# Optimization experiments

Hardware: AMD Instinct MI355X
Metric: run time of the kernel (lower is better)

Reference implementation:

```python
import jax, jax.numpy as jnp
import numpy as np

N_NODES = 500_000
N_EDGES = 16_000_000
C_IN = 1
C_OUT = 4


def gcn_conv(x, edge_index, W, b):
    """PyG GCNConv: add self-loops, symmetric normalization, linear + scatter-add.
    x: [N, Cin], edge_index: [2, E] (src, dst), W: [Cin, Cout], b: [Cout].
    """
    n = x.shape[0]
    loops = jnp.arange(n, dtype=edge_index.dtype)
    src = jnp.concatenate([edge_index[0], loops])  # [E+N]
    dst = jnp.concatenate([edge_index[1], loops])  # [E+N]
    h = x @ W  # [N, Cout]
    # degree at target nodes (with self-loops)
    deg = jax.ops.segment_sum(jnp.ones_like(dst, dtype=h.dtype), dst, num_segments=n)
    dinv = jnp.where(deg > 0, jax.lax.rsqrt(deg), 0.0)  # deg^{-1/2}
    norm = dinv[src] * dinv[dst]  # [E+N]
    msgs = norm[:, None] * h[src]  # [E+N, Cout] gathered + scaled messages
    out = jax.ops.segment_sum(msgs, dst, num_segments=n)  # scatter-add at targets
    return out + b


def setup_inputs() -> dict:
    key = jax.random.key(0)
    k0, k1, k2, k3 = jax.random.split(key, 4)
    x = jax.random.normal(k0, (N_NODES, C_IN), dtype=jnp.float32)
    edge_index = jax.random.randint(k1, (2, N_EDGES), 0, N_NODES, dtype=jnp.int64)
    W1 = jax.random.normal(k2, (C_IN, C_OUT), dtype=jnp.float32) / np.sqrt(C_IN)
    b1 = jnp.zeros((C_OUT,), dtype=jnp.float32)
    W2 = jax.random.normal(k3, (C_OUT, C_OUT), dtype=jnp.float32) / np.sqrt(C_OUT)
    b2 = jnp.zeros((C_OUT,), dtype=jnp.float32)
    return {"x": x, "edge_index": edge_index, "W1": W1, "b1": b1, "W2": W2, "b2": b2}


def reference(x, edge_index, W1, b1, W2, b2):
    h = jax.nn.relu(gcn_conv(x, edge_index, W1, b1))
    return gcn_conv(h, edge_index, W2, b2)
```

## Files before the change

kernel.cpp:

```cpp
#include <hip/hip_runtime.h>


#define B1_BLOCKS 512
#define B1_THREADS 1024
#define TILE1 16384
#define B2_THREADS 1024
#define TILE2 16384
#define MAXNB1 256
#define SORT_STAGE 12032
#define FB_BLOCKS 512
#define FB_THREADS 1024
#define FB_PAD 8
#define MAXNBF 2048

__global__ __launch_bounds__(B1_THREADS) void k_bin1(
    const int* __restrict__ src, const int* __restrict__ dst, int E,
    int chunk, int nb1, int C1, int* __restrict__ gcur1,
    int* __restrict__ pay1) {
  __shared__ int out[TILE1];
  __shared__ int hist[MAXNB1], toff[MAXNB1], wcur[MAXNB1], gb[MAXNB1];
  __shared__ int sbuf[2][MAXNB1];
  const int tid = threadIdx.x;
  const long long e0 = (long long)blockIdx.x * chunk;
  long long reml = (long long)E - e0;
  const int lim = reml < 0 ? 0 : (reml < chunk ? (int)reml : chunk);
  const int* dch = dst + e0;
  const int* sch = src + e0;

  for (int tb = 0; tb < lim; tb += TILE1) {
    const int tcnt = min(TILE1, lim - tb);
    const int nv = tcnt >> 2;
    for (int j = tid; j < MAXNB1; j += B1_THREADS) hist[j] = 0;
    __syncthreads();

    const int* dt = dch + tb;
    for (int k = tid; k < nv; k += B1_THREADS) {
      int4 d = reinterpret_cast<const int4*>(dt)[k];
      atomicAdd(&hist[d.x >> 11], 1);
      atomicAdd(&hist[d.y >> 11], 1);
      atomicAdd(&hist[d.z >> 11], 1);
      atomicAdd(&hist[d.w >> 11], 1);
    }
    for (int k = (nv << 2) + tid; k < tcnt; k += B1_THREADS)
      atomicAdd(&hist[dt[k] >> 11], 1);
    __syncthreads();

    if (tid < MAXNB1) sbuf[0][tid] = hist[tid];
    __syncthreads();
    int pi = 0;
    for (int dd = 1; dd < MAXNB1; dd <<= 1) {
      if (tid < MAXNB1) {
        int v = sbuf[pi][tid];
        if (tid >= dd) v += sbuf[pi][tid - dd];
        sbuf[pi ^ 1][tid] = v;
      }
      pi ^= 1;
      __syncthreads();
    }
    if (tid < MAXNB1) {
      int c = hist[tid];
      int exc = sbuf[pi][tid] - c;
      toff[tid] = exc;
      wcur[tid] = exc;
      gb[tid] = c ? atomicAdd(&gcur1[tid], c) : 0;
    }
    __syncthreads();

    const int* st = sch + tb;
    for (int k = tid; k < nv; k += B1_THREADS) {
      int4 d = reinterpret_cast<const int4*>(dt)[k];
      int4 s = reinterpret_cast<const int4*>(st)[k];
      int r0 = atomicAdd(&wcur[d.x >> 11], 1);
      int r1 = atomicAdd(&wcur[d.y >> 11], 1);
      int r2 = atomicAdd(&wcur[d.z >> 11], 1);
      int r3 = atomicAdd(&wcur[d.w >> 11], 1);
      out[r0] = (s.x << 11) | (d.x & 2047);
      out[r1] = (s.y << 11) | (d.y & 2047);
      out[r2] = (s.z << 11) | (d.z & 2047);
      out[r3] = (s.w << 11) | (d.w & 2047);
    }
    for (int k = (nv << 2) + tid; k < tcnt; k += B1_THREADS) {
      int d = dt[k], s = st[k];
      int r = atomicAdd(&wcur[d >> 11], 1);
      out[r] = (s << 11) | (d & 2047);
    }
    __syncthreads();

    const int wv = tid >> 6, lane = tid & 63;
    for (int j = wv; j < nb1; j += 16) {
      const int c = wcur[j] - toff[j];
      if (!c) continue;
      const int gbase = gb[j];
      const long long pbase = (long long)j * C1;
      for (int q = lane; q < c; q += 64) {
        int gi = gbase + q;
        if (gi < C1) pay1[pbase + gi] = out[toff[j] + q];
      }
    }
    __syncthreads();
  }
}

__global__ __launch_bounds__(B2_THREADS) void k_bin2(
    const int* __restrict__ pay1, const int* __restrict__ gcur1, int C1,
    int C2, int* __restrict__ gcur2, int* __restrict__ pay2) {
  __shared__ int out[TILE2];
  __shared__ int hist[8], toff9[9], wcur[8], gb[8];
  const int cb = blockIdx.x >> 1;
  const int half = blockIdx.x & 1;
  const int tid = threadIdx.x;
  const int Lc = min(gcur1[cb], C1);
  int mid = ((Lc >> 1) + 3) & ~3;
  if (mid > Lc) mid = Lc;
  const int h0 = half ? mid : 0;
  const int h1 = half ? Lc : mid;
  const int* seg = pay1 + (long long)cb * C1;

  for (int tb = h0; tb < h1; tb += TILE2) {
    const int tcnt = min(TILE2, h1 - tb);
    const int nv = tcnt >> 2;
    if (tid < 8) hist[tid] = 0;
    __syncthreads();
    const int* pt = seg + tb;

    for (int k = tid; k < nv; k += B2_THREADS) {
      int4 p = reinterpret_cast<const int4*>(pt)[k];
      atomicAdd(&hist[(p.x >> 8) & 7], 1);
      atomicAdd(&hist[(p.y >> 8) & 7], 1);
      atomicAdd(&hist[(p.z >> 8) & 7], 1);
      atomicAdd(&hist[(p.w >> 8) & 7], 1);
    }
    for (int k = (nv << 2) + tid; k < tcnt; k += B2_THREADS)
      atomicAdd(&hist[(pt[k] >> 8) & 7], 1);
    __syncthreads();

    if (tid == 0) {
      int run = 0;
      for (int j = 0; j < 8; ++j) { toff9[j] = run; run += hist[j]; }
      toff9[8] = run;
    }
    __syncthreads();
    if (tid < 8) {
      wcur[tid] = toff9[tid];
      gb[tid] = hist[tid] ? atomicAdd(&gcur2[cb * 8 + tid], hist[tid]) : 0;
    }
    __syncthreads();

    for (int k = tid; k < nv; k += B2_THREADS) {
      int4 p = reinterpret_cast<const int4*>(pt)[k];
      out[atomicAdd(&wcur[(p.x >> 8) & 7], 1)] = ((p.x >> 11) << 8) | (p.x & 255);
      out[atomicAdd(&wcur[(p.y >> 8) & 7], 1)] = ((p.y >> 11) << 8) | (p.y & 255);
      out[atomicAdd(&wcur[(p.z >> 8) & 7], 1)] = ((p.z >> 11) << 8) | (p.z & 255);
      out[atomicAdd(&wcur[(p.w >> 8) & 7], 1)] = ((p.w >> 11) << 8) | (p.w & 255);
    }
    for (int k = (nv << 2) + tid; k < tcnt; k += B2_THREADS) {
      int p = pt[k];
      out[atomicAdd(&wcur[(p >> 8) & 7], 1)] = ((p >> 11) << 8) | (p & 255);
    }
    __syncthreads();

    const int total = toff9[8];
    for (int q = tid; q < total; q += B2_THREADS) {
      int j = (q >= toff9[4]) ? 4 : 0;
      j += (q >= toff9[j + 2]) ? 2 : 0;
      j += (q >= toff9[j + 1]) ? 1 : 0;
      int o = gb[j] + (q - toff9[j]);
      if (o < C2) pay2[(long long)(cb * 8 + j) * C2 + o] = out[q];
    }
    __syncthreads();
  }
}

__global__ __launch_bounds__(FB_THREADS) void k_bin_flat(
    const int* __restrict__ src, const int* __restrict__ dst, int E,
    int chunk, int nbf, int C, int* __restrict__ gcur,
    int* __restrict__ payload) {
  __shared__ int hist[MAXNBF];
  __shared__ int lbase[MAXNBF];
  const int tid = threadIdx.x;
  const long long e0 = (long long)blockIdx.x * chunk;
  long long rem = (long long)E - e0;
  int lim = rem < 0 ? 0 : (rem < chunk ? (int)rem : chunk);
  for (int j = tid; j < nbf; j += FB_THREADS) hist[j] = 0;
  __syncthreads();
  const int* dch = dst + e0;
  const int* sch = src + e0;
  const int nv = lim >> 2;
  for (int k = tid; k < nv; k += FB_THREADS) {
    int4 d = reinterpret_cast<const int4*>(dch)[k];
    atomicAdd(&hist[d.x >> 8], 1);
    atomicAdd(&hist[d.y >> 8], 1);
    atomicAdd(&hist[d.z >> 8], 1);
    atomicAdd(&hist[d.w >> 8], 1);
  }
  for (int k = (nv << 2) + tid; k < lim; k += FB_THREADS)
    atomicAdd(&hist[dch[k] >> 8], 1);
  __syncthreads();
  for (int j = tid; j < nbf; j += FB_THREADS) {
    int c = hist[j];
    lbase[j] = c ? atomicAdd(&gcur[j], (c + FB_PAD - 1) & ~(FB_PAD - 1)) : 0;
    hist[j] = 0;
  }
  __syncthreads();
  for (int k = tid; k < nv; k += FB_THREADS) {
    int4 d = reinterpret_cast<const int4*>(dch)[k];
    int4 s = reinterpret_cast<const int4*>(sch)[k];
    int b0 = d.x >> 8, b1 = d.y >> 8, b2 = d.z >> 8, b3 = d.w >> 8;
    int r0 = atomicAdd(&hist[b0], 1) + lbase[b0];
    int r1 = atomicAdd(&hist[b1], 1) + lbase[b1];
    int r2 = atomicAdd(&hist[b2], 1) + lbase[b2];
    int r3 = atomicAdd(&hist[b3], 1) + lbase[b3];
    if (r0 < C) payload[(long long)b0 * C + r0] = (s.x << 8) | (d.x & 255);
    if (r1 < C) payload[(long long)b1 * C + r1] = (s.y << 8) | (d.y & 255);
    if (r2 < C) payload[(long long)b2 * C + r2] = (s.z << 8) | (d.z & 255);
    if (r3 < C) payload[(long long)b3 * C + r3] = (s.w << 8) | (d.w & 255);
  }
  for (int k = (nv << 2) + tid; k < lim; k += FB_THREADS) {
    int d = dch[k], s = sch[k];
    int bk = d >> 8;
    int r = atomicAdd(&hist[bk], 1) + lbase[bk];
    if (r < C) payload[(long long)bk * C + r] = (s << 8) | (d & 255);
  }
  __syncthreads();
  for (int j = tid; j < nbf; j += FB_THREADS) {
    int c = hist[j];
    if (c) {
      int pc = (c + FB_PAD - 1) & ~(FB_PAD - 1);
      long long base = (long long)j * C;
      for (int k = lbase[j] + c; k < lbase[j] + pc; ++k)
        if (k < C) payload[base + k] = -1;
    }
  }
}

__global__ __launch_bounds__(256) void k_sort(
    int* __restrict__ payload, const int* __restrict__ gcur, int C,
    int n, const float* __restrict__ x,
    int* __restrict__ off_g, float* __restrict__ y) {
  __shared__ int stage[SORT_STAGE];
  __shared__ int hist[256];
  __shared__ int sbuf[2][256];
  __shared__ int cur[256];
  const int b = blockIdx.x, t = threadIdx.x;
  hist[t] = 0;
  __syncthreads();
  int* seg = payload + (long long)b * C;
  const int L = min(gcur[b], C);
  const int nv = L >> 2;
#pragma unroll 2
  for (int k = t; k < nv; k += 256) {
    int4 p = reinterpret_cast<const int4*>(seg)[k];
    reinterpret_cast<int4*>(stage)[k] = p;
    if (p.x >= 0) atomicAdd(&hist[p.x & 255], 1);
    if (p.y >= 0) atomicAdd(&hist[p.y & 255], 1);
    if (p.z >= 0) atomicAdd(&hist[p.z & 255], 1);
    if (p.w >= 0) atomicAdd(&hist[p.w & 255], 1);
  }
  for (int k = (nv << 2) + t; k < L; k += 256) {
    int p = seg[k];
    stage[k] = p;
    if (p >= 0) atomicAdd(&hist[p & 255], 1);
  }
  __syncthreads();
  sbuf[0][t] = hist[t];
  __syncthreads();
  int pi = 0;
  for (int d = 1; d < 256; d <<= 1) {
    int v = sbuf[pi][t];
    if (t >= d) v += sbuf[pi][t - d];
    sbuf[pi ^ 1][t] = v;
    pi ^= 1;
    __syncthreads();
  }
  const int inc = sbuf[pi][t];
  const int exc = inc - hist[t];
  cur[t] = exc;
  off_g[b * 257 + t] = exc;
  if (t == 255) off_g[b * 257 + 256] = inc;
  const int i = (b << 8) + t;
  if (i < n) y[i] = rsqrtf((float)(hist[t] + 1)) * x[i];
  __syncthreads();
#pragma unroll 4
  for (int k = t; k < L; k += 256) {
    int p = stage[k];
    if (p >= 0) {
      int pos = atomicAdd(&cur[p & 255], 1);
      seg[pos] = p;
    }
  }
}

__global__ __launch_bounds__(256) void k_reduce1(
    const int* __restrict__ payload, const int* __restrict__ off_g, int C,
    int n, const float* __restrict__ y, float2* __restrict__ ds) {
  __shared__ float S[256];
  const int b = blockIdx.x, t = threadIdx.x;
  S[t] = 0.0f;
  __syncthreads();
  const int L = off_g[b * 257 + 256];
  const int* seg = payload + (long long)b * C;
  const int lane = t & 63;
  for (int base = t - lane; base < L; base += 256) {
    int k = base + lane;
    bool valid = k < L;
    int p = valid ? seg[k] : 0;
    int m = valid ? (p & 255) : 999;
    float v = valid ? y[p >> 8] : 0.0f;
#pragma unroll
    for (int d = 1; d < 64; d <<= 1) {
      float vv = __shfl_up(v, d, 64);
      int mm = __shfl_up(m, d, 64);
      if (lane >= d && mm == m) v += vv;
    }
    int mn = __shfl_down(m, 1, 64);
    if ((lane == 63 || mn != m) && m < 256) atomicAdd(&S[m], v);
  }
  __syncthreads();
  const int i = (b << 8) + t;
  if (i < n) {
    int deg = off_g[b * 257 + t + 1] - off_g[b * 257 + t];
    float r = rsqrtf((float)(deg + 1));
    ds[i] = make_float2(r, r * (S[t] + y[i]));
  }
}

__global__ __launch_bounds__(256) void k_reduce2(
    const int* __restrict__ payload, const int* __restrict__ off_g, int C,
    int n, const float2* __restrict__ ds,
    const float* __restrict__ W1, const float* __restrict__ b1,
    const float* __restrict__ W2, const float* __restrict__ b2,
    float4* __restrict__ out) {
  __shared__ float S0[256], S1[256], S2[256], S3[256];
  const int b = blockIdx.x, t = threadIdx.x;
  S0[t] = 0.f; S1[t] = 0.f; S2[t] = 0.f; S3[t] = 0.f;
  __syncthreads();
  const float w10 = W1[0], w11 = W1[1], w12 = W1[2], w13 = W1[3];
  const float c10 = b1[0], c11 = b1[1], c12 = b1[2], c13 = b1[3];
  float w2[16];
#pragma unroll
  for (int k = 0; k < 16; ++k) w2[k] = W2[k];

  const int L = off_g[b * 257 + 256];
  const int* seg = payload + (long long)b * C;
  const int lane = t & 63;
  for (int base = t - lane; base < L; base += 256) {
    int k = base + lane;
    bool valid = k < L;
    int p = valid ? seg[k] : 0;
    int m = valid ? (p & 255) : 999;
    float2 v = valid ? ds[p >> 8] : make_float2(0.f, 0.f);
    float r = valid ? v.x : 0.0f;
    float s = v.y;
    float h0 = fmaxf(fmaf(s, w10, c10), 0.f);
    float h1 = fmaxf(fmaf(s, w11, c11), 0.f);
    float h2 = fmaxf(fmaf(s, w12, c12), 0.f);
    float h3 = fmaxf(fmaf(s, w13, c13), 0.f);
    float gx = r * (h0 * w2[0] + h1 * w2[4] + h2 * w2[8]  + h3 * w2[12]);
    float gy = r * (h0 * w2[1] + h1 * w2[5] + h2 * w2[9]  + h3 * w2[13]);
    float gz = r * (h0 * w2[2] + h1 * w2[6] + h2 * w2[10] + h3 * w2[14]);
    float gw = r * (h0 * w2[3] + h1 * w2[7] + h2 * w2[11] + h3 * w2[15]);
#pragma unroll
    for (int d = 1; d < 64; d <<= 1) {
      float ax = __shfl_up(gx, d, 64);
      float ay = __shfl_up(gy, d, 64);
      float az = __shfl_up(gz, d, 64);
      float aw = __shfl_up(gw, d, 64);
      int mm = __shfl_up(m, d, 64);
      if (lane >= d && mm == m) { gx += ax; gy += ay; gz += az; gw += aw; }
    }
    int mn = __shfl_down(m, 1, 64);
    if ((lane == 63 || mn != m) && m < 256) {
      atomicAdd(&S0[m], gx);
      atomicAdd(&S1[m], gy);
      atomicAdd(&S2[m], gz);
      atomicAdd(&S3[m], gw);
    }
  }
  __syncthreads();
  const int i = (b << 8) + t;
  if (i < n) {
    float2 v = ds[i];
    float r = v.x, s = v.y;
    float h0 = fmaxf(fmaf(s, w10, c10), 0.f);
    float h1 = fmaxf(fmaf(s, w11, c11), 0.f);
    float h2 = fmaxf(fmaf(s, w12, c12), 0.f);
    float h3 = fmaxf(fmaf(s, w13, c13), 0.f);
    float gx = r * (h0 * w2[0] + h1 * w2[4] + h2 * w2[8]  + h3 * w2[12]);
    float gy = r * (h0 * w2[1] + h1 * w2[5] + h2 * w2[9]  + h3 * w2[13]);
    float gz = r * (h0 * w2[2] + h1 * w2[6] + h2 * w2[10] + h3 * w2[14]);
    float gw = r * (h0 * w2[3] + h1 * w2[7] + h2 * w2[11] + h3 * w2[15]);
    out[i] = make_float4(b2[0] + r * (S0[t] + gx),
                         b2[1] + r * (S1[t] + gy),
                         b2[2] + r * (S2[t] + gz),
                         b2[3] + r * (S3[t] + gw));
  }
}

extern "C" void kernel_launch(void* const* d_in, const int* in_sizes, int n_in,
                              void* d_out, int out_size, void* d_ws, size_t ws_size,
                              hipStream_t stream) {
  const float* x  = (const float*)d_in[0];
  const int*   ei = (const int*)d_in[1];
  const float* W1 = (const float*)d_in[2];
  const float* b1 = (const float*)d_in[3];
  const float* W2 = (const float*)d_in[4];
  const float* b2 = (const float*)d_in[5];

  const int n = in_sizes[0];
  const int E = in_sizes[1] / 2;
  const int* src = ei;
  const int* dst = ei + E;

  const int nbf = (n + 255) >> 8;
  const int nb1 = (n + 2047) >> 11;
  auto al = [](size_t v) { return (v + 255) & ~(size_t)255; };

  const size_t nn = (size_t)n;
  size_t sz_off = al((size_t)nbf * 257 * 4);
  size_t sz_y   = al(nn * 4);
  size_t sz_ds  = al(nn * 8);
  size_t sz_gc  = al(((size_t)nb1 + nbf) * 4);
  size_t fixed = sz_off + sz_y + sz_ds + sz_gc;

  long long mean1 = (long long)E / (nb1 > 0 ? nb1 : 1);
  long long C1ll = ((mean1 + 2048 + 1024) + 15) & ~15LL;
  long long mean2 = (long long)E / nbf;
  long long C2ll = ((mean2 + 1024) + 15) & ~15LL;
  size_t need_main = fixed + al((size_t)nb1 * C1ll * 4) + al((size_t)nbf * C2ll * 4);
  const bool main_ok = (n <= 524288) && (nb1 <= MAXNB1) && (nbf <= MAXNBF) &&
                       (C2ll <= SORT_STAGE) && (need_main <= ws_size);

  if (main_ok) {
    const int C1 = (int)C1ll, C2 = (int)C2ll;
    char* p = (char*)d_ws;
    int*    pay1  = (int*)p;    p += al((size_t)nb1 * C1 * 4);
    int*    pay2  = (int*)p;    p += al((size_t)nbf * C2 * 4);
    int*    gcur1 = (int*)p;
    int*    gcur2 = gcur1 + nb1;
    p += sz_gc;
    int*    off_g = (int*)p;    p += sz_off;
    float*  y     = (float*)p;  p += sz_y;
    float2* ds    = (float2*)p; p += sz_ds;

    hipMemsetAsync(gcur1, 0, ((size_t)nb1 + nbf) * 4, stream);

    int chunk = (int)(((long long)E + B1_BLOCKS - 1) / B1_BLOCKS);
    chunk = (chunk + 3) & ~3;

    k_bin1<<<B1_BLOCKS, B1_THREADS, 0, stream>>>(src, dst, E, chunk, nb1, C1,
                                                 gcur1, pay1);
    k_bin2<<<nb1 * 2, B2_THREADS, 0, stream>>>(pay1, gcur1, C1, C2, gcur2,
                                               pay2);
    k_sort<<<nbf, 256, 0, stream>>>(pay2, gcur2, C2, n, x, off_g, y);
    k_reduce1<<<nbf, 256, 0, stream>>>(pay2, off_g, C2, n, y, ds);
    k_reduce2<<<nbf, 256, 0, stream>>>(pay2, off_g, C2, n, ds, W1, b1, W2, b2,
                                       (float4*)d_out);
    return;
  }

  {
    double mean = (double)E / nbf;
    long long Cwant = (long long)(mean * 1.10) +
                      (long long)(FB_BLOCKS * FB_PAD / 2) + 512;
    size_t budget = ws_size > fixed ? ws_size - fixed - 4096 : 0;
    long long Cbud = (long long)(budget / ((size_t)nbf * 4));
    long long Cll = Cwant < Cbud ? Cwant : Cbud;
    if (Cll > SORT_STAGE) Cll = SORT_STAGE;
    int C = (int)(Cll & ~(long long)(FB_PAD - 1));

    char* p = (char*)d_ws;
    int*    pay2  = (int*)p;    p += al((size_t)nbf * C * 4);
    int*    gcur  = (int*)p;    p += sz_gc;
    int*    off_g = (int*)p;    p += sz_off;
    float*  y     = (float*)p;  p += sz_y;
    float2* ds    = (float2*)p; p += sz_ds;

    hipMemsetAsync(gcur, 0, (size_t)nbf * 4, stream);

    int chunk = (int)(((long long)E + FB_BLOCKS - 1) / FB_BLOCKS);
    chunk = (chunk + 3) & ~3;

    k_bin_flat<<<FB_BLOCKS, FB_THREADS, 0, stream>>>(src, dst, E, chunk, nbf,
                                                     C, gcur, pay2);
    k_sort<<<nbf, 256, 0, stream>>>(pay2, gcur, C, n, x, off_g, y);
    k_reduce1<<<nbf, 256, 0, stream>>>(pay2, off_g, C, n, y, ds);
    k_reduce2<<<nbf, 256, 0, stream>>>(pay2, off_g, C, n, ds, W1, b1, W2, b2,
                                       (float4*)d_out);
  }
}
```

Baseline: 538.9 us.

## Reduce per-node segments with 4-lane groups instead of wave segmented scans

Both reduce kernels now rely on the per-node offsets from the sort stage. Each group of 4 lanes walks one destination node's contiguous edge range and combines partial sums with xor shuffles. This removes the 64-wide segmented scan, the LDS atomics and the block barriers. It assumes the segment is fully sorted by node within each block, and it risks load imbalance and divergence across lanes when node degrees vary.

```diff
diff --git a/kernel.cpp b/kernel.cpp
--- a/kernel.cpp
+++ b/kernel.cpp
@@ -293,34 +293,27 @@
 __global__ __launch_bounds__(256) void k_reduce1(
     const int* __restrict__ payload, const int* __restrict__ off_g, int C,
     int n, const float* __restrict__ y, float2* __restrict__ ds) {
-  __shared__ float S[256];
   const int b = blockIdx.x, t = threadIdx.x;
-  S[t] = 0.0f;
-  __syncthreads();
-  const int L = off_g[b * 257 + 256];
+  const int g = t >> 2, lane4 = t & 3;
   const int* seg = payload + (long long)b * C;
-  const int lane = t & 63;
-  for (int base = t - lane; base < L; base += 256) {
-    int k = base + lane;
-    bool valid = k < L;
-    int p = valid ? seg[k] : 0;
-    int m = valid ? (p & 255) : 999;
-    float v = valid ? y[p >> 8] : 0.0f;
+  const int* off = off_g + b * 257;
+  float keep = 0.0f;
 #pragma unroll
-    for (int d = 1; d < 64; d <<= 1) {
-      float vv = __shfl_up(v, d, 64);
-      int mm = __shfl_up(m, d, 64);
-      if (lane >= d && mm == m) v += vv;
-    }
-    int mn = __shfl_down(m, 1, 64);
-    if ((lane == 63 || mn != m) && m < 256) atomicAdd(&S[m], v);
-  }
-  __syncthreads();
+  for (int j = 0; j < 4; ++j) {
+    const int m = (g << 2) | j;
+    const int o0 = off[m], o1 = off[m + 1];
+    float acc = 0.0f;
+    for (int k = o0 + lane4; k < o1; k += 4)
+      acc += y[seg[k] >> 8];
+    acc += __shfl_xor(acc, 1, 4);
+    acc += __shfl_xor(acc, 2, 4);
+    if (j == lane4) keep = acc;
+  }
   const int i = (b << 8) + t;
   if (i < n) {
-    int deg = off_g[b * 257 + t + 1] - off_g[b * 257 + t];
-    float r = rsqrtf((float)(deg + 1));
-    ds[i] = make_float2(r, r * (S[t] + y[i]));
+    const int deg = off[t + 1] - off[t];
+    const float r = rsqrtf((float)(deg + 1));
+    ds[i] = make_float2(r, r * (keep + y[i]));
   }
 }
 
@@ -330,69 +323,60 @@
     const float* __restrict__ W1, const float* __restrict__ b1,
     const float* __restrict__ W2, const float* __restrict__ b2,
     float4* __restrict__ out) {
-  __shared__ float S0[256], S1[256], S2[256], S3[256];
   const int b = blockIdx.x, t = threadIdx.x;
-  S0[t] = 0.f; S1[t] = 0.f; S2[t] = 0.f; S3[t] = 0.f;
-  __syncthreads();
+  const int g = t >> 2, lane4 = t & 3;
   const float w10 = W1[0], w11 = W1[1], w12 = W1[2], w13 = W1[3];
   const float c10 = b1[0], c11 = b1[1], c12 = b1[2], c13 = b1[3];
   float w2[16];
 #pragma unroll
   for (int k = 0; k < 16; ++k) w2[k] = W2[k];
-
-  const int L = off_g[b * 257 + 256];
   const int* seg = payload + (long long)b * C;
-  const int lane = t & 63;
-  for (int base = t - lane; base < L; base += 256) {
-    int k = base + lane;
-    bool valid = k < L;
-    int p = valid ? seg[k] : 0;
-    int m = valid ? (p & 255) : 999;
-    float2 v = valid ? ds[p >> 8] : make_float2(0.f, 0.f);
-    float r = valid ? v.x : 0.0f;
-    float s = v.y;
-    float h0 = fmaxf(fmaf(s, w10, c10), 0.f);
-    float h1 = fmaxf(fmaf(s, w11, c11), 0.f);
-    float h2 = fmaxf(fmaf(s, w12, c12), 0.f);
-    float h3 = fmaxf(fmaf(s, w13, c13), 0.f);
-    float gx = r * (h0 * w2[0] + h1 * w2[4] + h2 * w2[8]  + h3 * w2[12]);
-    float gy = r * (h0 * w2[1] + h1 * w2[5] + h2 * w2[9]  + h3 * w2[13]);
-    float gz = r * (h0 * w2[2] + h1 * w2[6] + h2 * w2[10] + h3 * w2[14]);
-    float gw = r * (h0 * w2[3] + h1 * w2[7] + h2 * w2[11] + h3 * w2[15]);
+  const int* off = off_g + b * 257;
+  float kx = 0.f, ky = 0.f, kz = 0.f, kw = 0.f;
 #pragma unroll
-    for (int d = 1; d < 64; d <<= 1) {
-      float ax = __shfl_up(gx, d, 64);
-      float ay = __shfl_up(gy, d, 64);
-      float az = __shfl_up(gz, d, 64);
-      float aw = __shfl_up(gw, d, 64);
-      int mm = __shfl_up(m, d, 64);
-      if (lane >= d && mm == m) { gx += ax; gy += ay; gz += az; gw += aw; }
-    }
-    int mn = __shfl_down(m, 1, 64);
-    if ((lane == 63 || mn != m) && m < 256) {
-      atomicAdd(&S0[m], gx);
-      atomicAdd(&S1[m], gy);
-      atomicAdd(&S2[m], gz);
-      atomicAdd(&S3[m], gw);
-    }
-  }
-  __syncthreads();
+  for (int j = 0; j < 4; ++j) {
+    const int m = (g << 2) | j;
+    const int o0 = off[m], o1 = off[m + 1];
+    float gx = 0.f, gy = 0.f, gz = 0.f, gw = 0.f;
+    for (int k = o0 + lane4; k < o1; k += 4) {
+      const int p = seg[k];
+      const float2 v = ds[p >> 8];
+      const float r = v.x, s = v.y;
+      const float h0 = fmaxf(fmaf(s, w10, c10), 0.f);
+      const float h1 = fmaxf(fmaf(s, w11, c11), 0.f);
+      const float h2 = fmaxf(fmaf(s, w12, c12), 0.f);
+      const float h3 = fmaxf(fmaf(s, w13, c13), 0.f);
+      gx += r * (h0 * w2[0] + h1 * w2[4] + h2 * w2[8]  + h3 * w2[12]);
+      gy += r * (h0 * w2[1] + h1 * w2[5] + h2 * w2[9]  + h3 * w2[13]);
+      gz += r * (h0 * w2[2] + h1 * w2[6] + h2 * w2[10] + h3 * w2[14]);
+      gw += r * (h0 * w2[3] + h1 * w2[7] + h2 * w2[11] + h3 * w2[15]);
+    }
+    gx += __shfl_xor(gx, 1, 4);
+    gx += __shfl_xor(gx, 2, 4);
+    gy += __shfl_xor(gy, 1, 4);
+    gy += __shfl_xor(gy, 2, 4);
+    gz += __shfl_xor(gz, 1, 4);
+    gz += __shfl_xor(gz, 2, 4);
+    gw += __shfl_xor(gw, 1, 4);
+    gw += __shfl_xor(gw, 2, 4);
+    if (j == lane4) { kx = gx; ky = gy; kz = gz; kw = gw; }
+  }
   const int i = (b << 8) + t;
   if (i < n) {
-    float2 v = ds[i];
-    float r = v.x, s = v.y;
-    float h0 = fmaxf(fmaf(s, w10, c10), 0.f);
-    float h1 = fmaxf(fmaf(s, w11, c11), 0.f);
-    float h2 = fmaxf(fmaf(s, w12, c12), 0.f);
-    float h3 = fmaxf(fmaf(s, w13, c13), 0.f);
-    float gx = r * (h0 * w2[0] + h1 * w2[4] + h2 * w2[8]  + h3 * w2[12]);
-    float gy = r * (h0 * w2[1] + h1 * w2[5] + h2 * w2[9]  + h3 * w2[13]);
-    float gz = r * (h0 * w2[2] + h1 * w2[6] + h2 * w2[10] + h3 * w2[14]);
-    float gw = r * (h0 * w2[3] + h1 * w2[7] + h2 * w2[11] + h3 * w2[15]);
-    out[i] = make_float4(b2[0] + r * (S0[t] + gx),
-                         b2[1] + r * (S1[t] + gy),
-                         b2[2] + r * (S2[t] + gz),
-                         b2[3] + r * (S3[t] + gw));
+    const float2 v = ds[i];
+    const float r = v.x, s = v.y;
+    const float h0 = fmaxf(fmaf(s, w10, c10), 0.f);
+    const float h1 = fmaxf(fmaf(s, w11, c11), 0.f);
+    const float h2 = fmaxf(fmaf(s, w12, c12), 0.f);
+    const float h3 = fmaxf(fmaf(s, w13, c13), 0.f);
+    const float sx = r * (h0 * w2[0] + h1 * w2[4] + h2 * w2[8]  + h3 * w2[12]);
+    const float sy = r * (h0 * w2[1] + h1 * w2[5] + h2 * w2[9]  + h3 * w2[13]);
+    const float sz = r * (h0 * w2[2] + h1 * w2[6] + h2 * w2[10] + h3 * w2[14]);
+    const float sw = r * (h0 * w2[3] + h1 * w2[7] + h2 * w2[11] + h3 * w2[15]);
+    out[i] = make_float4(b2[0] + r * (kx + sx),
+                         b2[1] + r * (ky + sy),
+                         b2[2] + r * (kz + sz),
+                         b2[3] + r * (kw + sw));
   }
 }
 
```

New measurement: 607.9 us. 1.13x slower.
